# Performance work log

Measured on AMD Instinct MI355X. Metric: run time of the kernel, lower is better.

The kernel has to match this reference:

```python
import jax, jax.numpy as jnp
import numpy as np

NEG = -9e15
ALPHA = 0.2  # leaky relu slope


def _gat_layer(x, adj, W, a_src, a_tgt, concat):
    # x: [N, F_in], W: [H, F_in, F_out], a_src/a_tgt: [H, 1, F_out]
    Wh = jnp.einsum('nf,hfo->hno', x, W)                      # [H, N, F_out]
    s_i = jnp.sum(a_src * Wh, axis=2, keepdims=True)          # [H, N, 1]
    s_j = jnp.sum(a_tgt * Wh, axis=2, keepdims=True)          # [H, N, 1]
    e = jax.nn.leaky_relu(s_i + jnp.swapaxes(s_j, 1, 2), ALPHA)  # [H, N, N]
    e = jnp.where(adj > 0, e, NEG)
    attn = jax.nn.softmax(e, axis=2)                          # [H, N, N]
    h = jnp.einsum('hnm,hmo->hno', attn, Wh)                  # [H, N, F_out]
    if concat:
        H, N, F = h.shape
        return jnp.transpose(h, (1, 0, 2)).reshape(N, H * F)
    return h.mean(axis=0)


def setup_inputs() -> dict:
    key = jax.random.key(0)
    ks = jax.random.split(key, 8)
    N, F_in, Hid, H1, C = 6000, 512, 64, 8, 40
    return {
        'x': jax.random.normal(ks[0], (N, F_in), jnp.float32),
        'adj': jax.random.randint(ks[1], (N, N), 0, 2, jnp.int32),
        'W1': jax.random.normal(ks[2], (H1, F_in, Hid), jnp.float32) * 0.05,
        'a_src1': jax.random.normal(ks[3], (H1, 1, Hid), jnp.float32) * 0.1,
        'a_tgt1': jax.random.normal(ks[4], (H1, 1, Hid), jnp.float32) * 0.1,
        'W2': jax.random.normal(ks[5], (1, H1 * Hid, C), jnp.float32) * 0.05,
        'a_src2': jax.random.normal(ks[6], (1, 1, C), jnp.float32) * 0.1,
        'a_tgt2': jax.random.normal(ks[7], (1, 1, C), jnp.float32) * 0.1,
    }


def reference(x, adj, W1, a_src1, a_tgt1, W2, a_src2, a_tgt2):
    # Layer 1: 8 heads, concat, ELU activation
    h = _gat_layer(x, adj, W1, a_src1, a_tgt1, concat=True)   # [N, 8*64]
    h = jax.nn.elu(h)
    # Final layer: 1 head, mean over heads, no activation
    out = _gat_layer(h, adj, W2, a_src2, a_tgt2, concat=False)  # [N, 40]
    return (out, adj)
```

## Files before the change

kernel.cpp:

```cpp
#include <hip/hip_runtime.h>
#include <hip/hip_bf16.h>
#include <stdint.h>

#define GN   6000
#define GNP2 3000
#define GFIN 512
#define GNH  8
#define GNC  40
#define WPR  192
#define NT   192
#define NRT  375
#define PQS  6144
#define PQH  (PQS/2)
#define KC1  8
#define CW1  24
#define KC2  32
#define CW2  6

typedef __attribute__((ext_vector_type(8))) _Float16 half8v;
typedef __attribute__((ext_vector_type(2))) _Float16 half2v;
typedef __attribute__((ext_vector_type(4))) float float4v;
typedef __attribute__((ext_vector_type(4))) float f32x4;

__device__ __forceinline__ uint32_t packh(float a, float b){
  half2v h = { (_Float16)a, (_Float16)b };
  return *(uint32_t*)&h;
}
__device__ __forceinline__ float h2lo(uint32_t u){ half2v h = *(half2v*)&u; return (float)h.x; }
__device__ __forceinline__ float h2hi(uint32_t u){ half2v h = *(half2v*)&u; return (float)h.y; }
__device__ __forceinline__ int kmap(int g, int t){
  return (t < 2) ? 4*g + 2*t : 16 + 4*g + 2*(t - 2);
}
__device__ __forceinline__ int newpos(int gg, int c){
  return (gg < 4) ? 8*gg + c : 8*(gg-4) + 4 + c;
}

__global__ void k_prep(const float* __restrict__ as2, const float* __restrict__ at2,
                       float* __restrict__ as2f, float* __restrict__ at2f,
                       uint32_t* __restrict__ Wt1, uint32_t* __restrict__ Wt2,
                       uint32_t* __restrict__ pk1, uint32_t* __restrict__ qk1,
                       uint32_t* __restrict__ pk2, uint32_t* __restrict__ qk2){
  int i = blockIdx.x * 256 + threadIdx.x;
  if (i < 64) { as2f[i] = (i < GNC) ? as2[i] : 0.f; at2f[i] = (i < GNC) ? at2[i] : 0.f; }
  if (i < GNH*PQH) { pk1[i] = 0u; qk1[i] = 0u; }
  if (i < PQH) { pk2[i] = 0u; qk2[i] = 0u; }
  if (i < GNH*5*1024) {
    int h = i / 5120, rem = i - h * 5120;
    Wt1[((size_t)h*NT + 187)*1024 + rem] = 0u;
  }
  if (i < 5*1024) Wt2[(size_t)187*1024 + i] = 0u;
}

__global__ void k_bitmask(const int* __restrict__ adj, uint32_t* __restrict__ bm){
  int idx = blockIdx.x * 256 + threadIdx.x;
  if (idx >= GN * WPR) return;
  int row = idx / WPR, w = idx - row * WPR;
  int j0 = w * 32;
  uint32_t bits = 0u;
  if (j0 < GN) {
    const int* a = adj + (size_t)row * GN + j0;
    int lim = GN - j0;
    if (lim >= 32) {
      const int4* a4 = (const int4*)a;
      #pragma unroll
      for (int gg = 0; gg < 8; ++gg) {
        int4 v = a4[gg];
        bits |= (v.x != 0 ? 1u : 0u) << newpos(gg, 0);
        bits |= (v.y != 0 ? 1u : 0u) << newpos(gg, 1);
        bits |= (v.z != 0 ? 1u : 0u) << newpos(gg, 2);
        bits |= (v.w != 0 ? 1u : 0u) << newpos(gg, 3);
      }
    } else {
      for (int b = 0; b < lim; ++b)
        bits |= (a[b] != 0 ? 1u : 0u) << newpos(b >> 2, b & 3);
    }
  }
  bm[idx] = bits;
}

__global__ void k_xtile(const float* __restrict__ x, uint32_t* __restrict__ xt){
  int idx = blockIdx.x * 256 + threadIdx.x;
  int e = idx & 3, lane = (idx >> 2) & 63, kt = (idx >> 8) & 15, rt = idx >> 12;
  int g = lane >> 4, r = lane & 15;
  int k0 = kt*32 + kmap(g, e);
  const float* xp = x + (size_t)(rt*16 + r) * GFIN + k0;
  xt[idx] = packh(xp[0], xp[1]);
}

__global__ void k_wtile1(const float* __restrict__ W1, uint32_t* __restrict__ Wb1){
  int idx = blockIdx.x * 256 + threadIdx.x;
  int e = idx & 3, lane = (idx >> 2) & 63, n = (idx >> 8) & 3, kt = (idx >> 10) & 15, h = idx >> 14;
  int g = lane >> 4, col = n*16 + (lane & 15);
  int k0 = kt*32 + kmap(g, e);
  const float* wp = W1 + ((size_t)h*GFIN + k0) * 64 + col;
  Wb1[idx] = packh(wp[0], wp[64]);
}

__global__ void k_wtile2(const float* __restrict__ W2, uint32_t* __restrict__ Wb2){
  int idx = blockIdx.x * 256 + threadIdx.x;
  int e = idx & 3, lane = (idx >> 2) & 63, n = (idx >> 8) & 3, kt = idx >> 10;
  int g = lane >> 4, col = n*16 + (lane & 15);
  int k0 = kt*32 + kmap(g, e);
  float v0 = (col < GNC) ? W2[(size_t)k0*GNC + col]     : 0.f;
  float v1 = (col < GNC) ? W2[(size_t)(k0+1)*GNC + col] : 0.f;
  Wb2[idx] = packh(v0, v1);
}

__global__ __launch_bounds__(256) void k_gemm_mfma(
    const uint32_t* __restrict__ At, const uint32_t* __restrict__ Bt,
    const float* __restrict__ asv, const float* __restrict__ atv,
    uint32_t* __restrict__ Wt, float* __restrict__ ss, float* __restrict__ st,
    int ones_col){
  int lane = threadIdx.x & 63;
  int wid  = threadIdx.x >> 6;
  int h  = blockIdx.y;
  int rt = blockIdx.x * 4 + wid;
  if (rt >= NRT) return;
  int g = lane >> 4, r = lane & 15;
  const uint32_t* Ab = At + (size_t)rt * 16 * 256 + lane * 4;
  const uint32_t* Bb = Bt + (size_t)h * 16 * 1024 + lane * 4;
  float4v acc[4];
  #pragma unroll
  for (int n = 0; n < 4; ++n) acc[n] = (float4v){0,0,0,0};
  for (int kt = 0; kt < 16; ++kt) {
    union { uint4 v; half8v hv; } A;
    A.v = *(const uint4*)(Ab + kt*256);
    #pragma unroll
    for (int n = 0; n < 4; ++n) {
      union { uint4 v; half8v hv; } B;
      B.v = *(const uint4*)(Bb + kt*1024 + n*256);
      acc[n] = __builtin_amdgcn_mfma_f32_16x16x32_f16(A.hv, B.hv, acc[n], 0, 0, 0);
    }
  }
  int row0 = rt * 16;
  int t01  = (row0 & 16) ? 2 : 0;
  uint32_t* dst = Wt + ((size_t)h*NT + (row0 >> 5)) * 1024 + lane*4 + t01;
  #pragma unroll
  for (int n = 0; n < 4; ++n) {
    uint2 val;
    if (n*16 + r == ones_col) val = make_uint2(0x3C003C00u, 0x3C003C00u);
    else val = make_uint2(packh(acc[n][0], acc[n][1]), packh(acc[n][2], acc[n][3]));
    *(uint2*)(dst + n*256) = val;
  }
  float av[4], tv[4];
  #pragma unroll
  for (int n = 0; n < 4; ++n) { av[n] = asv[h*64 + n*16 + r]; tv[n] = atv[h*64 + n*16 + r]; }
  #pragma unroll
  for (int reg = 0; reg < 4; ++reg) {
    float a = 0.f, b = 0.f;
    #pragma unroll
    for (int n = 0; n < 4; ++n) { a = fmaf(av[n], acc[n][reg], a); b = fmaf(tv[n], acc[n][reg], b); }
    #pragma unroll
    for (int d = 1; d < 16; d <<= 1) { a += __shfl_xor(a, d, 64); b += __shfl_xor(b, d, 64); }
    if (r == 0) {
      ss[(size_t)h*GN + row0 + 4*g + reg] = a;
      st[(size_t)h*GN + row0 + 4*g + reg] = b;
    }
  }
}

__global__ void k_stats(const float* __restrict__ s_tgt, float* __restrict__ mh_out,
                        uint32_t* __restrict__ ppk, uint32_t* __restrict__ qpk){
  int h = blockIdx.x;
  __shared__ float red[256];
  float mx = -3.0e38f;
  for (int n = threadIdx.x; n < GN; n += 256) mx = fmaxf(mx, s_tgt[(size_t)h*GN + n]);
  red[threadIdx.x] = mx;
  __syncthreads();
  for (int d = 128; d > 0; d >>= 1) {
    if (threadIdx.x < d) red[threadIdx.x] = fmaxf(red[threadIdx.x], red[threadIdx.x + d]);
    __syncthreads();
  }
  float mh = red[0];
  if (threadIdx.x == 0) mh_out[h] = mh;
  for (int jp = threadIdx.x; jp < GNP2; jp += 256) {
    float s0 = s_tgt[(size_t)h*GN + 2*jp];
    float s1 = s_tgt[(size_t)h*GN + 2*jp + 1];
    ppk[(size_t)h*PQH + jp] = packh(expf(s0 - mh), expf(s1 - mh));
    qpk[(size_t)h*PQH + jp] = packh(expf(0.2f*(s0 - mh)), expf(0.2f*(s1 - mh)));
  }
}

template<int CW, int NH, int KC, int NTILES, bool ONES>
__global__ __launch_bounds__(256) void k_attn_t(
    const uint32_t* __restrict__ bmp, const uint32_t* __restrict__ Wt,
    const float* __restrict__ ss, const float* __restrict__ mh_arr,
    const uint32_t* __restrict__ ppk, const uint32_t* __restrict__ qpk,
    uint32_t* __restrict__ part, float* __restrict__ Zp){
  int lane = threadIdx.x & 63;
  int wid  = threadIdx.x >> 6;
  constexpr int NB = NH * KC;
  int combo = blockIdx.x % NB;
  int x     = blockIdx.x / NB;
  int h  = combo / KC;
  int ch = combo % KC;
  int base = x * 256 + wid * 64;
  int g = lane >> 4, r = lane & 15;
  float mh = mh_arr[h];
  const uint32_t* bmr[4];
  uint32_t ti2u[4];
  #pragma unroll
  for (int tt = 0; tt < 4; ++tt) {
    int row = base + 16*tt + r;
    int rc = row < GN-1 ? row : GN-1;
    float si = ss[(size_t)h*GN + rc];
    float ti = expf(-0.8f * (si + mh));
    ti2u[tt] = packh(ti, ti);
    bmr[tt] = bmp + (size_t)rc * WPR;
  }
  const uint32_t* pph = ppk + (size_t)h * PQH;
  const uint32_t* qqh = qpk + (size_t)h * PQH;
  const uint32_t* wt  = Wt + (size_t)h * NT * 1024;
  float4v acc[4][NTILES];
  float4v az[4];
  #pragma unroll
  for (int tt = 0; tt < 4; ++tt) {
    #pragma unroll
    for (int n = 0; n < NTILES; ++n) acc[tt][n] = (float4v){0,0,0,0};
    if (ONES) az[tt] = (float4v){0,0,0,0};
  }
  union { uint32_t u4[4]; half8v hv; } Bones;
  if (ONES) {
    uint32_t ov = (r == 0) ? 0x3C003C00u : 0u;
    Bones.u4[0] = ov; Bones.u4[1] = ov; Bones.u4[2] = ov; Bones.u4[3] = ov;
  }
  const int w0 = ch * CW;
  for (int wp = 0; wp < CW/2; ++wp) {
    uint2 bw2[4];
    #pragma unroll
    for (int tt = 0; tt < 4; ++tt) bw2[tt] = *(const uint2*)(bmr[tt] + w0 + 2*wp);
    #pragma unroll
    for (int e = 0; e < 2; ++e) {
      int w = w0 + 2*wp + e;
      int jp = w * 16;
      uint2 pA = *(const uint2*)(pph + jp + 2*g);
      uint2 pB = *(const uint2*)(pph + jp + 8 + 2*g);
      uint2 qA = *(const uint2*)(qqh + jp + 2*g);
      uint2 qB = *(const uint2*)(qqh + jp + 8 + 2*g);
      uint32_t pd[4] = {pA.x, pA.y, pB.x, pB.y};
      uint32_t qd[4] = {qA.x, qA.y, qB.x, qB.y};
      const uint32_t* tb = wt + (size_t)w * 1024 + lane * 4;
      union { uint4 v; half8v hv; } B[NTILES];
      #pragma unroll
      for (int n = 0; n < NTILES; ++n) B[n].v = *(const uint4*)(tb + n*256);
      #pragma unroll
      for (int tt = 0; tt < 4; ++tt) {
        uint32_t bw = e ? bw2[tt].y : bw2[tt].x;
        uint32_t b8 = (bw >> (8*g)) & 0xFFu;
        union { uint32_t u4[4]; half8v hv; } A;
        #pragma unroll
        for (int t = 0; t < 4; ++t) {
          uint32_t prod, wvu;
          asm("v_pk_mul_f16 %0, %1, %2" : "=v"(prod) : "v"(ti2u[tt]), "v"(qd[t]));
          asm("v_pk_max_f16 %0, %1, %2" : "=v"(wvu) : "v"(pd[t]), "v"(prod));
          int32_t ma = ((int32_t)(b8 << (31 - 2*t))) >> 31;
          int32_t mb = ((int32_t)(b8 << (30 - 2*t))) >> 31;
          uint32_t m = ((uint32_t)ma & 0x0000FFFFu) | ((uint32_t)mb & 0xFFFF0000u);
          A.u4[t] = wvu & m;
        }
        #pragma unroll
        for (int n = 0; n < NTILES; ++n)
          acc[tt][n] = __builtin_amdgcn_mfma_f32_16x16x32_f16(A.hv, B[n].hv, acc[tt][n], 0, 0, 0);
        if (ONES)
          az[tt] = __builtin_amdgcn_mfma_f32_16x16x32_f16(A.hv, Bones.hv, az[tt], 0, 0, 0);
      }
    }
  }
  constexpr int PST = NTILES * 16;
  size_t pb = ((size_t)(ch * NH + h)) * GNP2;
  #pragma unroll
  for (int tt = 0; tt < 4; ++tt) {
    int row0t = base + 16*tt;
    if (row0t >= GN) break;
    int pra = (row0t >> 1) + 2*g;
    #pragma unroll
    for (int n = 0; n < NTILES; ++n) {
      part[(pb + pra    )*PST + n*16 + r] = packh(acc[tt][n][0], acc[tt][n][1]);
      part[(pb + pra + 1)*PST + n*16 + r] = packh(acc[tt][n][2], acc[tt][n][3]);
    }
    if (ONES && r == 0) {
      size_t zb = ((size_t)(ch * NH + h)) * GN;
      #pragma unroll
      for (int reg = 0; reg < 4; ++reg) Zp[zb + row0t + 4*g + reg] = az[tt][reg];
    }
  }
}

__global__ void k_reduce1(const uint32_t* __restrict__ part1, const float* __restrict__ Zp1,
                          uint32_t* __restrict__ h1t){
  int idx = blockIdx.x * 256 + threadIdx.x;
  if (idx >= GNH*GNP2*64) return;
  int o = idx & 63;
  int t = idx >> 6;
  int pr = t % GNP2;
  int h = t / GNP2;
  float s0 = 0.f, s1 = 0.f, z0 = 0.f, z1 = 0.f;
  #pragma unroll
  for (int c = 0; c < KC1; ++c) {
    uint32_t dw = part1[(((size_t)(c*GNH + h))*GNP2 + pr)*64 + o];
    s0 += h2lo(dw);
    s1 += h2hi(dw);
    size_t zb = ((size_t)(c*GNH + h))*GN + 2*pr;
    z0 += Zp1[zb]; z1 += Zp1[zb + 1];
  }
  float v0 = s0 / z0, v1 = s1 / z1;
  v0 = v0 > 0.f ? v0 : (expf(v0) - 1.f);
  v1 = v1 > 0.f ? v1 : (expf(v1) - 1.f);
  int n0 = 2*pr;
  int rt = n0 >> 4, rr = n0 & 15;
  int k = h*64 + o;
  int kt = k >> 5, joff = k & 31;
  int g, tt, b;
  if (joff < 16) { g = joff >> 2; tt = (joff & 3) >> 1;        b = joff & 1; }
  else { int jo = joff - 16; g = jo >> 2; tt = 2 + ((jo & 3) >> 1); b = jo & 1; }
  size_t dw0 = ((size_t)(rt*16 + kt))*256 + (g*16 + rr)*4 + tt;
  _Float16* hp = (_Float16*)h1t;
  hp[dw0*2 + b]     = (_Float16)v0;
  hp[(dw0+4)*2 + b] = (_Float16)v1;
}

__global__ void k_reduce2(const uint32_t* __restrict__ part2, float* __restrict__ out){
  int idx = blockIdx.x * 256 + threadIdx.x;
  if (idx >= GN * GNC) return;
  int n = idx / GNC, c = idx - n * GNC;
  int pr = n >> 1, half = n & 1;
  float s = 0.f, z = 0.f;
  #pragma unroll 8
  for (int ch = 0; ch < KC2; ++ch) {
    const uint32_t* row = part2 + ((size_t)ch * GNP2 + pr) * 48;
    uint32_t dS = row[c], dZ = row[47];
    s += half ? h2hi(dS) : h2lo(dS);
    z += half ? h2hi(dZ) : h2lo(dZ);
  }
  out[idx] = s / z;
}

__global__ void k_echo(const uint32_t* __restrict__ bm, float* __restrict__ echo){
  int idx = blockIdx.x * 256 + threadIdx.x;
  if (idx >= GN * 1500) return;
  int row = idx / 1500, c = idx - row * 1500;
  uint32_t bits = bm[(size_t)row * WPR + (c >> 3)];
  int gg = c & 7;
  f32x4 f;
  f.x = ((bits >> newpos(gg,0)) & 1u) ? 1.f : 0.f;
  f.y = ((bits >> newpos(gg,1)) & 1u) ? 1.f : 0.f;
  f.z = ((bits >> newpos(gg,2)) & 1u) ? 1.f : 0.f;
  f.w = ((bits >> newpos(gg,3)) & 1u) ? 1.f : 0.f;
  *(f32x4*)(echo + (size_t)idx * 4) = f;
}

extern "C" void kernel_launch(void* const* d_in, const int* in_sizes, int n_in,
                              void* d_out, int out_size, void* d_ws, size_t ws_size,
                              hipStream_t stream){
  const float* x   = (const float*)d_in[0];
  const int*   adj = (const int*)d_in[1];
  const float* W1  = (const float*)d_in[2];
  const float* as1 = (const float*)d_in[3];
  const float* at1 = (const float*)d_in[4];
  const float* W2  = (const float*)d_in[5];
  const float* as2 = (const float*)d_in[6];
  const float* at2 = (const float*)d_in[7];
  float* out  = (float*)d_out;
  float* echo = out + (size_t)GN * GNC;
  (void)in_sizes; (void)n_in; (void)out_size; (void)ws_size;

  uint32_t* part1u = (uint32_t*)echo;
  float*    Zp1    = (float*)(part1u + (size_t)KC1*GNH*GNP2*64);
  uint32_t* part2u = (uint32_t*)(Zp1 + (size_t)KC1*GNH*GN);
  uint32_t* h1t    = part2u + (size_t)KC2*GNP2*48;
  uint32_t* xt     = h1t + (size_t)NRT*16*256;

  char* wsb = (char*)d_ws;
  size_t off = 0;
  auto alloc = [&](size_t bytes) -> void* {
    void* r = wsb + off;
    off = (off + bytes + 255) & ~(size_t)255;
    return r;
  };
  uint32_t* bmp  = (uint32_t*)alloc((size_t)GN * WPR * 4);
  uint32_t* Wt1  = (uint32_t*)alloc((size_t)GNH * NT * 1024 * 4);
  uint32_t* Wt2  = (uint32_t*)alloc((size_t)NT * 1024 * 4);
  uint32_t* Wb1  = (uint32_t*)alloc((size_t)GNH * 16 * 1024 * 4);
  uint32_t* Wb2  = (uint32_t*)alloc((size_t)16 * 1024 * 4);
  float*    as2f = (float*)alloc(64 * 4);
  float*    at2f = (float*)alloc(64 * 4);
  float*    ss1  = (float*)alloc((size_t)GNH * GN * 4);
  float*    st1  = (float*)alloc((size_t)GNH * GN * 4);
  uint32_t* pk1  = (uint32_t*)alloc((size_t)GNH * PQH * 4);
  uint32_t* qk1  = (uint32_t*)alloc((size_t)GNH * PQH * 4);
  float*    m1   = (float*)alloc(64);
  float*    ss2  = (float*)alloc((size_t)GN * 4);
  float*    st2  = (float*)alloc((size_t)GN * 4);
  uint32_t* pk2  = (uint32_t*)alloc((size_t)PQH * 4);
  uint32_t* qk2  = (uint32_t*)alloc((size_t)PQH * 4);
  float*    m2   = (float*)alloc(64);

  const int NX = (GN + 255) / 256;

  hipLaunchKernelGGL(k_prep, dim3(192), dim3(256), 0, stream,
      as2, at2, as2f, at2f, Wt1, Wt2, pk1, qk1, pk2, qk2);
  hipLaunchKernelGGL(k_bitmask, dim3(GN*WPR/256), dim3(256), 0, stream, adj, bmp);
  hipLaunchKernelGGL(k_xtile, dim3(NRT*16*256/256), dim3(256), 0, stream, x, xt);
  hipLaunchKernelGGL(k_wtile1, dim3(512), dim3(256), 0, stream, W1, Wb1);
  hipLaunchKernelGGL(k_wtile2, dim3(64), dim3(256), 0, stream, W2, Wb2);
  hipLaunchKernelGGL(k_gemm_mfma, dim3((NRT+3)/4, GNH), dim3(256), 0, stream,
      xt, Wb1, as1, at1, Wt1, ss1, st1, -1);
  hipLaunchKernelGGL(k_stats, dim3(GNH), dim3(256), 0, stream, st1, m1, pk1, qk1);
  hipLaunchKernelGGL((k_attn_t<CW1, GNH, KC1, 4, true>), dim3(NX * GNH * KC1), dim3(256), 0, stream,
      bmp, Wt1, ss1, m1, pk1, qk1, part1u, Zp1);
  hipLaunchKernelGGL(k_reduce1, dim3(GNH*GNP2*64/256), dim3(256), 0, stream,
      part1u, Zp1, h1t);
  hipLaunchKernelGGL(k_gemm_mfma, dim3((NRT+3)/4, 1), dim3(256), 0, stream,
      h1t, Wb2, as2f, at2f, Wt2, ss2, st2, 47);
  hipLaunchKernelGGL(k_stats, dim3(1), dim3(256), 0, stream, st2, m2, pk2, qk2);
  hipLaunchKernelGGL((k_attn_t<CW2, 1, KC2, 3, false>), dim3(NX * KC2), dim3(256), 0, stream,
      bmp, Wt2, ss2, m2, pk2, qk2, part2u, (float*)nullptr);
  hipLaunchKernelGGL(k_reduce2, dim3((GN*GNC+255)/256), dim3(256), 0, stream,
      part2u, out);
  hipLaunchKernelGGL(k_echo, dim3((GN*1500+255)/256), dim3(256), 0, stream, bmp, echo);
}
```

Before: 230.8 us.

## Restructure layer-1 attention to share bitmask masks across four heads per wave

```diff
diff --git a/kernel.cpp b/kernel.cpp
--- a/kernel.cpp
+++ b/kernel.cpp
@@ -34,16 +34,27 @@
 __device__ __forceinline__ int newpos(int gg, int c){
   return (gg < 4) ? 8*gg + c : 8*(gg-4) + 4 + c;
 }
+__device__ __forceinline__ uint32_t wvbuild(uint32_t ti2, uint32_t pq_q, uint32_t pq_p, uint32_t m){
+  uint32_t prod, wvu;
+  asm("v_pk_mul_f16 %0, %1, %2" : "=v"(prod) : "v"(ti2), "v"(pq_q));
+  asm("v_pk_max_f16 %0, %1, %2" : "=v"(wvu) : "v"(pq_p), "v"(prod));
+  return wvu & m;
+}
+__device__ __forceinline__ uint32_t mbuild(uint32_t b8, int t, uint32_t s15){
+  uint32_t pre = (b8 << (15 - 2*t)) | (b8 << (30 - 2*t));
+  uint32_t m;
+  asm("v_pk_ashrrev_i16 %0, %1, %2" : "=v"(m) : "v"(s15), "v"(pre));
+  return m;
+}
 
 __global__ void k_prep(const float* __restrict__ as2, const float* __restrict__ at2,
                        float* __restrict__ as2f, float* __restrict__ at2f,
                        uint32_t* __restrict__ Wt1, uint32_t* __restrict__ Wt2,
-                       uint32_t* __restrict__ pk1, uint32_t* __restrict__ qk1,
-                       uint32_t* __restrict__ pk2, uint32_t* __restrict__ qk2){
+                       uint32_t* __restrict__ pqk1, uint32_t* __restrict__ pqk2){
   int i = blockIdx.x * 256 + threadIdx.x;
   if (i < 64) { as2f[i] = (i < GNC) ? as2[i] : 0.f; at2f[i] = (i < GNC) ? at2[i] : 0.f; }
-  if (i < GNH*PQH) { pk1[i] = 0u; qk1[i] = 0u; }
-  if (i < PQH) { pk2[i] = 0u; qk2[i] = 0u; }
+  if (i < GNH*PQH*2) pqk1[i] = 0u;
+  if (i < PQH*2) pqk2[i] = 0u;
   if (i < GNH*5*1024) {
     int h = i / 5120, rem = i - h * 5120;
     Wt1[((size_t)h*NT + 187)*1024 + rem] = 0u;
@@ -160,7 +171,7 @@
 }
 
 __global__ void k_stats(const float* __restrict__ s_tgt, float* __restrict__ mh_out,
-                        uint32_t* __restrict__ ppk, uint32_t* __restrict__ qpk){
+                        uint32_t* __restrict__ pqk){
   int h = blockIdx.x;
   __shared__ float red[256];
   float mx = -3.0e38f;
@@ -176,56 +187,154 @@
   for (int jp = threadIdx.x; jp < GNP2; jp += 256) {
     float s0 = s_tgt[(size_t)h*GN + 2*jp];
     float s1 = s_tgt[(size_t)h*GN + 2*jp + 1];
-    ppk[(size_t)h*PQH + jp] = packh(expf(s0 - mh), expf(s1 - mh));
-    qpk[(size_t)h*PQH + jp] = packh(expf(0.2f*(s0 - mh)), expf(0.2f*(s1 - mh)));
-  }
-}
-
-template<int CW, int NH, int KC, int NTILES, bool ONES>
-__global__ __launch_bounds__(256) void k_attn_t(
+    pqk[((size_t)h*PQH + jp)*2]     = packh(expf(s0 - mh), expf(s1 - mh));
+    pqk[((size_t)h*PQH + jp)*2 + 1] = packh(expf(0.2f*(s0 - mh)), expf(0.2f*(s1 - mh)));
+  }
+}
+
+__global__ __launch_bounds__(256) void k_attn1mh(
     const uint32_t* __restrict__ bmp, const uint32_t* __restrict__ Wt,
     const float* __restrict__ ss, const float* __restrict__ mh_arr,
-    const uint32_t* __restrict__ ppk, const uint32_t* __restrict__ qpk,
+    const uint32_t* __restrict__ pqk,
     uint32_t* __restrict__ part, float* __restrict__ Zp){
   int lane = threadIdx.x & 63;
   int wid  = threadIdx.x >> 6;
-  constexpr int NB = NH * KC;
-  int combo = blockIdx.x % NB;
-  int x     = blockIdx.x / NB;
-  int h  = combo / KC;
-  int ch = combo % KC;
+  int ch = blockIdx.x % KC1;
+  int x  = blockIdx.x / KC1;
+  int base = x * 64 + (wid & 1) * 32;
+  int hg   = (wid >> 1) * 4;
+  int g = lane >> 4, r = lane & 15;
+  uint32_t s15 = 0x000F000Fu;
+  int ra = base + r, rb = ra + 16;
+  int rac = ra < GN-1 ? ra : GN-1;
+  int rbc = rb < GN-1 ? rb : GN-1;
+  uint32_t tiA[4], tiB[4];
+  const uint32_t* pqh[4];
+  const uint32_t* wtl[4];
+  #pragma unroll
+  for (int u = 0; u < 4; ++u) {
+    int h = hg + u;
+    float mh = mh_arr[h];
+    float ta = expf(-0.8f * (ss[(size_t)h*GN + rac] + mh));
+    float tb = expf(-0.8f * (ss[(size_t)h*GN + rbc] + mh));
+    tiA[u] = packh(ta, ta);
+    tiB[u] = packh(tb, tb);
+    pqh[u] = pqk + (size_t)h * PQH * 2;
+    wtl[u] = Wt + (size_t)h * NT * 1024 + lane * 4;
+  }
+  const uint32_t* bma = bmp + (size_t)rac * WPR;
+  const uint32_t* bmb = bmp + (size_t)rbc * WPR;
+  float4v accA[4][4], accB[4][4], azA[4], azB[4];
+  #pragma unroll
+  for (int u = 0; u < 4; ++u) {
+    #pragma unroll
+    for (int n = 0; n < 4; ++n) { accA[u][n] = (float4v){0,0,0,0}; accB[u][n] = (float4v){0,0,0,0}; }
+    azA[u] = (float4v){0,0,0,0}; azB[u] = (float4v){0,0,0,0};
+  }
+  union { uint32_t u4[4]; half8v hv; } Bones;
+  {
+    uint32_t ov = (r == 0) ? 0x3C003C00u : 0u;
+    Bones.u4[0] = ov; Bones.u4[1] = ov; Bones.u4[2] = ov; Bones.u4[3] = ov;
+  }
+  const int w0 = ch * CW1;
+  for (int wp = 0; wp < CW1/2; ++wp) {
+    uint2 bwa = *(const uint2*)(bma + w0 + 2*wp);
+    uint2 bwb = *(const uint2*)(bmb + w0 + 2*wp);
+    #pragma unroll
+    for (int e = 0; e < 2; ++e) {
+      int w = w0 + 2*wp + e;
+      int jp = w * 16;
+      uint32_t b8a = ((e ? bwa.y : bwa.x) >> (8*g)) & 0xFFu;
+      uint32_t b8b = ((e ? bwb.y : bwb.x) >> (8*g)) & 0xFFu;
+      uint32_t ma[4], mb[4];
+      #pragma unroll
+      for (int t = 0; t < 4; ++t) { ma[t] = mbuild(b8a, t, s15); mb[t] = mbuild(b8b, t, s15); }
+      #pragma unroll
+      for (int u = 0; u < 4; ++u) {
+        uint4 pqA = *(const uint4*)(pqh[u] + (size_t)(jp + 2*g) * 2);
+        uint4 pqB = *(const uint4*)(pqh[u] + (size_t)(jp + 8 + 2*g) * 2);
+        union { uint32_t u4[4]; half8v hv; } Aa, Ab;
+        Aa.u4[0] = wvbuild(tiA[u], pqA.y, pqA.x, ma[0]);
+        Aa.u4[1] = wvbuild(tiA[u], pqA.w, pqA.z, ma[1]);
+        Aa.u4[2] = wvbuild(tiA[u], pqB.y, pqB.x, ma[2]);
+        Aa.u4[3] = wvbuild(tiA[u], pqB.w, pqB.z, ma[3]);
+        Ab.u4[0] = wvbuild(tiB[u], pqA.y, pqA.x, mb[0]);
+        Ab.u4[1] = wvbuild(tiB[u], pqA.w, pqA.z, mb[1]);
+        Ab.u4[2] = wvbuild(tiB[u], pqB.y, pqB.x, mb[2]);
+        Ab.u4[3] = wvbuild(tiB[u], pqB.w, pqB.z, mb[3]);
+        const uint32_t* tb = wtl[u] + (size_t)w * 1024;
+        #pragma unroll
+        for (int n = 0; n < 4; ++n) {
+          union { uint4 v; half8v hv; } B;
+          B.v = *(const uint4*)(tb + n*256);
+          accA[u][n] = __builtin_amdgcn_mfma_f32_16x16x32_f16(Aa.hv, B.hv, accA[u][n], 0, 0, 0);
+          accB[u][n] = __builtin_amdgcn_mfma_f32_16x16x32_f16(Ab.hv, B.hv, accB[u][n], 0, 0, 0);
+        }
+        azA[u] = __builtin_amdgcn_mfma_f32_16x16x32_f16(Aa.hv, Bones.hv, azA[u], 0, 0, 0);
+        azB[u] = __builtin_amdgcn_mfma_f32_16x16x32_f16(Ab.hv, Bones.hv, azB[u], 0, 0, 0);
+      }
+    }
+  }
+  #pragma unroll
+  for (int u = 0; u < 4; ++u) {
+    int h = hg + u;
+    size_t pb = ((size_t)(ch * GNH + h)) * GNP2;
+    size_t zb = ((size_t)(ch * GNH + h)) * GN;
+    int pra = (base >> 1) + 2*g;
+    #pragma unroll
+    for (int n = 0; n < 4; ++n) {
+      part[(pb + pra    )*64 + n*16 + r] = packh(accA[u][n][0], accA[u][n][1]);
+      part[(pb + pra + 1)*64 + n*16 + r] = packh(accA[u][n][2], accA[u][n][3]);
+    }
+    if (r == 0) {
+      #pragma unroll
+      for (int reg = 0; reg < 4; ++reg) Zp[zb + base + 4*g + reg] = azA[u][reg];
+    }
+    if (base + 16 < GN) {
+      int prb = pra + 8;
+      #pragma unroll
+      for (int n = 0; n < 4; ++n) {
+        part[(pb + prb    )*64 + n*16 + r] = packh(accB[u][n][0], accB[u][n][1]);
+        part[(pb + prb + 1)*64 + n*16 + r] = packh(accB[u][n][2], accB[u][n][3]);
+      }
+      if (r == 0) {
+        #pragma unroll
+        for (int reg = 0; reg < 4; ++reg) Zp[zb + base + 16 + 4*g + reg] = azB[u][reg];
+      }
+    }
+  }
+}
+
+__global__ __launch_bounds__(256) void k_attn2n(
+    const uint32_t* __restrict__ bmp, const uint32_t* __restrict__ Wt,
+    const float* __restrict__ ss, const float* __restrict__ mh_arr,
+    const uint32_t* __restrict__ pqk, uint32_t* __restrict__ part){
+  int lane = threadIdx.x & 63;
+  int wid  = threadIdx.x >> 6;
+  int ch = blockIdx.x % KC2;
+  int x  = blockIdx.x / KC2;
   int base = x * 256 + wid * 64;
   int g = lane >> 4, r = lane & 15;
-  float mh = mh_arr[h];
+  uint32_t s15 = 0x000F000Fu;
+  float mh = mh_arr[0];
   const uint32_t* bmr[4];
   uint32_t ti2u[4];
   #pragma unroll
   for (int tt = 0; tt < 4; ++tt) {
     int row = base + 16*tt + r;
     int rc = row < GN-1 ? row : GN-1;
-    float si = ss[(size_t)h*GN + rc];
-    float ti = expf(-0.8f * (si + mh));
+    float ti = expf(-0.8f * (ss[rc] + mh));
     ti2u[tt] = packh(ti, ti);
     bmr[tt] = bmp + (size_t)rc * WPR;
   }
-  const uint32_t* pph = ppk + (size_t)h * PQH;
-  const uint32_t* qqh = qpk + (size_t)h * PQH;
-  const uint32_t* wt  = Wt + (size_t)h * NT * 1024;
-  float4v acc[4][NTILES];
-  float4v az[4];
-  #pragma unroll
-  for (int tt = 0; tt < 4; ++tt) {
-    #pragma unroll
-    for (int n = 0; n < NTILES; ++n) acc[tt][n] = (float4v){0,0,0,0};
-    if (ONES) az[tt] = (float4v){0,0,0,0};
-  }
-  union { uint32_t u4[4]; half8v hv; } Bones;
-  if (ONES) {
-    uint32_t ov = (r == 0) ? 0x3C003C00u : 0u;
-    Bones.u4[0] = ov; Bones.u4[1] = ov; Bones.u4[2] = ov; Bones.u4[3] = ov;
-  }
-  const int w0 = ch * CW;
-  for (int wp = 0; wp < CW/2; ++wp) {
+  const uint32_t* wtl = Wt + lane * 4;
+  float4v acc[4][3];
+  #pragma unroll
+  for (int tt = 0; tt < 4; ++tt)
+    #pragma unroll
+    for (int n = 0; n < 3; ++n) acc[tt][n] = (float4v){0,0,0,0};
+  const int w0 = ch * CW2;
+  for (int wp = 0; wp < CW2/2; ++wp) {
     uint2 bw2[4];
     #pragma unroll
     for (int tt = 0; tt < 4; ++tt) bw2[tt] = *(const uint2*)(bmr[tt] + w0 + 2*wp);
@@ -233,55 +342,36 @@
     for (int e = 0; e < 2; ++e) {
       int w = w0 + 2*wp + e;
       int jp = w * 16;
-      uint2 pA = *(const uint2*)(pph + jp + 2*g);
-      uint2 pB = *(const uint2*)(pph + jp + 8 + 2*g);
-      uint2 qA = *(const uint2*)(qqh + jp + 2*g);
-      uint2 qB = *(const uint2*)(qqh + jp + 8 + 2*g);
-      uint32_t pd[4] = {pA.x, pA.y, pB.x, pB.y};
-      uint32_t qd[4] = {qA.x, qA.y, qB.x, qB.y};
-      const uint32_t* tb = wt + (size_t)w * 1024 + lane * 4;
-      union { uint4 v; half8v hv; } B[NTILES];
-      #pragma unroll
-      for (int n = 0; n < NTILES; ++n) B[n].v = *(const uint4*)(tb + n*256);
+      uint4 pqA = *(const uint4*)(pqk + (size_t)(jp + 2*g) * 2);
+      uint4 pqB = *(const uint4*)(pqk + (size_t)(jp + 8 + 2*g) * 2);
+      const uint32_t* tb = wtl + (size_t)w * 1024;
+      union { uint4 v; half8v hv; } B[3];
+      #pragma unroll
+      for (int n = 0; n < 3; ++n) B[n].v = *(const uint4*)(tb + n*256);
       #pragma unroll
       for (int tt = 0; tt < 4; ++tt) {
-        uint32_t bw = e ? bw2[tt].y : bw2[tt].x;
-        uint32_t b8 = (bw >> (8*g)) & 0xFFu;
+        uint32_t b8 = ((e ? bw2[tt].y : bw2[tt].x) >> (8*g)) & 0xFFu;
         union { uint32_t u4[4]; half8v hv; } A;
+        A.u4[0] = wvbuild(ti2u[tt], pqA.y, pqA.x, mbuild(b8, 0, s15));
+        A.u4[1] = wvbuild(ti2u[tt], pqA.w, pqA.z, mbuild(b8, 1, s15));
+        A.u4[2] = wvbuild(ti2u[tt], pqB.y, pqB.x, mbuild(b8, 2, s15));
+        A.u4[3] = wvbuild(ti2u[tt], pqB.w, pqB.z, mbuild(b8, 3, s15));
         #pragma unroll
-        for (int t = 0; t < 4; ++t) {
-          uint32_t prod, wvu;
-          asm("v_pk_mul_f16 %0, %1, %2" : "=v"(prod) : "v"(ti2u[tt]), "v"(qd[t]));
-          asm("v_pk_max_f16 %0, %1, %2" : "=v"(wvu) : "v"(pd[t]), "v"(prod));
-          int32_t ma = ((int32_t)(b8 << (31 - 2*t))) >> 31;
-          int32_t mb = ((int32_t)(b8 << (30 - 2*t))) >> 31;
-          uint32_t m = ((uint32_t)ma & 0x0000FFFFu) | ((uint32_t)mb & 0xFFFF0000u);
-          A.u4[t] = wvu & m;
-        }
-        #pragma unroll
-        for (int n = 0; n < NTILES; ++n)
+        for (int n = 0; n < 3; ++n)
           acc[tt][n] = __builtin_amdgcn_mfma_f32_16x16x32_f16(A.hv, B[n].hv, acc[tt][n], 0, 0, 0);
-        if (ONES)
-          az[tt] = __builtin_amdgcn_mfma_f32_16x16x32_f16(A.hv, Bones.hv, az[tt], 0, 0, 0);
       }
     }
   }
-  constexpr int PST = NTILES * 16;
-  size_t pb = ((size_t)(ch * NH + h)) * GNP2;
+  size_t pb = (size_t)ch * GNP2;
   #pragma unroll
   for (int tt = 0; tt < 4; ++tt) {
     int row0t = base + 16*tt;
     if (row0t >= GN) break;
     int pra = (row0t >> 1) + 2*g;
     #pragma unroll
-    for (int n = 0; n < NTILES; ++n) {
-      part[(pb + pra    )*PST + n*16 + r] = packh(acc[tt][n][0], acc[tt][n][1]);
-      part[(pb + pra + 1)*PST + n*16 + r] = packh(acc[tt][n][2], acc[tt][n][3]);
-    }
-    if (ONES && r == 0) {
-      size_t zb = ((size_t)(ch * NH + h)) * GN;
-      #pragma unroll
-      for (int reg = 0; reg < 4; ++reg) Zp[zb + row0t + 4*g + reg] = az[tt][reg];
+    for (int n = 0; n < 3; ++n) {
+      part[(pb + pra    )*48 + n*16 + r] = packh(acc[tt][n][0], acc[tt][n][1]);
+      part[(pb + pra + 1)*48 + n*16 + r] = packh(acc[tt][n][2], acc[tt][n][3]);
     }
   }
 }
@@ -386,35 +476,31 @@
   float*    at2f = (float*)alloc(64 * 4);
   float*    ss1  = (float*)alloc((size_t)GNH * GN * 4);
   float*    st1  = (float*)alloc((size_t)GNH * GN * 4);
-  uint32_t* pk1  = (uint32_t*)alloc((size_t)GNH * PQH * 4);
-  uint32_t* qk1  = (uint32_t*)alloc((size_t)GNH * PQH * 4);
+  uint32_t* pqk1 = (uint32_t*)alloc((size_t)GNH * PQH * 2 * 4);
   float*    m1   = (float*)alloc(64);
   float*    ss2  = (float*)alloc((size_t)GN * 4);
   float*    st2  = (float*)alloc((size_t)GN * 4);
-  uint32_t* pk2  = (uint32_t*)alloc((size_t)PQH * 4);
-  uint32_t* qk2  = (uint32_t*)alloc((size_t)PQH * 4);
+  uint32_t* pqk2 = (uint32_t*)alloc((size_t)PQH * 2 * 4);
   float*    m2   = (float*)alloc(64);
 
-  const int NX = (GN + 255) / 256;
-
   hipLaunchKernelGGL(k_prep, dim3(192), dim3(256), 0, stream,
-      as2, at2, as2f, at2f, Wt1, Wt2, pk1, qk1, pk2, qk2);
+      as2, at2, as2f, at2f, Wt1, Wt2, pqk1, pqk2);
   hipLaunchKernelGGL(k_bitmask, dim3(GN*WPR/256), dim3(256), 0, stream, adj, bmp);
   hipLaunchKernelGGL(k_xtile, dim3(NRT*16*256/256), dim3(256), 0, stream, x, xt);
   hipLaunchKernelGGL(k_wtile1, dim3(512), dim3(256), 0, stream, W1, Wb1);
   hipLaunchKernelGGL(k_wtile2, dim3(64), dim3(256), 0, stream, W2, Wb2);
   hipLaunchKernelGGL(k_gemm_mfma, dim3((NRT+3)/4, GNH), dim3(256), 0, stream,
       xt, Wb1, as1, at1, Wt1, ss1, st1, -1);
-  hipLaunchKernelGGL(k_stats, dim3(GNH), dim3(256), 0, stream, st1, m1, pk1, qk1);
-  hipLaunchKernelGGL((k_attn_t<CW1, GNH, KC1, 4, true>), dim3(NX * GNH * KC1), dim3(256), 0, stream,
-      bmp, Wt1, ss1, m1, pk1, qk1, part1u, Zp1);
+  hipLaunchKernelGGL(k_stats, dim3(GNH), dim3(256), 0, stream, st1, m1, pqk1);
+  hipLaunchKernelGGL(k_attn1mh, dim3(94 * KC1), dim3(256), 0, stream,
+      bmp, Wt1, ss1, m1, pqk1, part1u, Zp1);
   hipLaunchKernelGGL(k_reduce1, dim3(GNH*GNP2*64/256), dim3(256), 0, stream,
       part1u, Zp1, h1t);
   hipLaunchKernelGGL(k_gemm_mfma, dim3((NRT+3)/4, 1), dim3(256), 0, stream,
       h1t, Wb2, as2f, at2f, Wt2, ss2, st2, 47);
-  hipLaunchKernelGGL(k_stats, dim3(1), dim3(256), 0, stream, st2, m2, pk2, qk2);
-  hipLaunchKernelGGL((k_attn_t<CW2, 1, KC2, 3, false>), dim3(NX * KC2), dim3(256), 0, stream,
-      bmp, Wt2, ss2, m2, pk2, qk2, part2u, (float*)nullptr);
+  hipLaunchKernelGGL(k_stats, dim3(1), dim3(256), 0, stream, st2, m2, pqk2);
+  hipLaunchKernelGGL(k_attn2n, dim3(24 * KC2), dim3(256), 0, stream,
+      bmp, Wt2, ss2, m2, pqk2, part2u);
   hipLaunchKernelGGL(k_reduce2, dim3((GN*GNC+255)/256), dim3(256), 0, stream,
       part2u, out);
   hipLaunchKernelGGL(k_echo, dim3((GN*1500+255)/256), dim3(256), 0, stream, bmp, echo);
```

After: 461.3 us. 99.9% more time.
